# Kernel optimization log

Measured on AMD Instinct MI355X. Metric: run time of the kernel, lower is better.

## Reference

```python
import jax, jax.numpy as jnp
import numpy as np

N = 100000   # nodes
E = 1600000  # edges
D_IN = 128
H = 64
L = 3        # num SAGE layers
G = 512      # graphs in batch


def setup_inputs() -> dict:
    key = jax.random.key(0)
    ks = jax.random.split(key, 12)
    s = 0.05
    return {
        "x": jax.random.normal(ks[0], (N, D_IN), dtype=jnp.float32),
        "edge_index": jax.random.randint(ks[1], (2, E), 0, N, dtype=jnp.int64),
        "edge_attr": jax.random.normal(ks[2], (E, 1), dtype=jnp.float32),
        "batch": jnp.sort(jax.random.randint(ks[3], (N,), 0, G, dtype=jnp.int64)),
        "W0": jax.random.normal(ks[4], (D_IN, H), dtype=jnp.float32) * s,
        "b0": jnp.zeros((H,), dtype=jnp.float32),
        "Wl": jax.random.normal(ks[5], (L, H, H), dtype=jnp.float32) * s,  # lin_l (aggregated neighbors), has bias
        "bl": jnp.zeros((L, H), dtype=jnp.float32),
        "Wr": jax.random.normal(ks[6], (L, H, H), dtype=jnp.float32) * s,  # lin_r (root), no bias
        "W1": jax.random.normal(ks[7], (H, H), dtype=jnp.float32) * s,
        "b1": jnp.zeros((H,), dtype=jnp.float32),
    }


def reference(x, edge_index, edge_attr, batch, W0, b0, Wl, bl, Wr, W1, b1):
    # edge_attr is accepted but unused, matching the torch module.
    h = jax.nn.relu(x @ W0 + b0)                    # [N, H]
    src, dst = edge_index[0], edge_index[1]
    ones_e = jnp.ones((E,), dtype=h.dtype)
    deg = jax.ops.segment_sum(ones_e, dst, num_segments=N)
    deg = jnp.clip(deg, 1.0)[:, None]               # avoid div by zero (PyG mean -> 0 for isolated)
    for i in range(L):
        # SAGEConv: mean-aggregate source features onto targets, then lin_l(agg)+lin_r(h)
        agg = jax.ops.segment_sum(h[src], dst, num_segments=N) / deg  # [N, H]
        h = jax.nn.relu(agg @ Wl[i] + bl[i] + h @ Wr[i])
    # global_mean_pool over batch ids
    cnt = jax.ops.segment_sum(jnp.ones((N,), dtype=h.dtype), batch, num_segments=G)
    pooled = jax.ops.segment_sum(h, batch, num_segments=G) / jnp.clip(cnt, 1.0)[:, None]  # [G, H]
    return pooled @ W1 + b1                          # [G, H]
```

## Files before the change

### kernel.cpp

```cpp
#include <hip/hip_runtime.h>
#include <hip/hip_bf16.h>

#define NN 100000
#define NE 1600000
#define DIN 128
#define NG 512
#define MAXD 64
#define NBUK 391
#define BCAP 5120
#define CHUNK ((NE + NBUK - 1) / NBUK)
#define NTILE ((NN + 63) >> 6)

typedef __attribute__((ext_vector_type(8))) __bf16 bf16x8;
typedef __attribute__((ext_vector_type(4))) float f32x4;

static __device__ __forceinline__ unsigned short bfhi(float f) {
    __hip_bfloat16 h = __float2bfloat16(f);
    return *reinterpret_cast<unsigned short*>(&h);
}
static __device__ __forceinline__ float bf2f(unsigned short u) {
    unsigned v = (unsigned)u << 16;
    return __uint_as_float(v);
}
static __device__ __forceinline__ bf16x8 ldfrag(const void* p) {
    bf16x8 r;
    __builtin_memcpy(&r, p, 16);
    return r;
}
static __device__ __forceinline__ int swz(int a) {
    return a ^ (((a >> 8) & 3) << 5) ^ (((a >> 12) & 3) << 4);
}


#define GB 256
__global__ void __launch_bounds__(512) k_front(const int* __restrict__ src,
                                               const int* __restrict__ dst,
                                               int* __restrict__ cursor,
                                               unsigned int* __restrict__ bucket,
                                               const float* __restrict__ x,
                                               const float* __restrict__ W0,
                                               const float* __restrict__ b0,
                                               float* __restrict__ h) {
    __shared__ unsigned short sA0[16 * 64 * 8];
    __shared__ unsigned short sA1[16 * 64 * 8];
    __shared__ unsigned short sB0[16 * 64 * 8];
    __shared__ unsigned short sB1[16 * 64 * 8];
    __shared__ int lcnt[NBUK];
    __shared__ int lbase[NBUK];
    if (blockIdx.x < NBUK) {
        for (int i = threadIdx.x; i < NBUK; i += 512) lcnt[i] = 0;
        __syncthreads();
        int e0 = blockIdx.x * CHUNK;
        int e1 = min(e0 + CHUNK, NE);
        for (int e = e0 + (int)threadIdx.x; e < e1; e += 512)
            atomicAdd(&lcnt[dst[e] >> 8], 1);
        __syncthreads();
        for (int i = threadIdx.x; i < NBUK; i += 512) {
            int c = lcnt[i];
            lbase[i] = c ? atomicAdd(&cursor[i], c) : 0;
            lcnt[i] = 0;
        }
        __syncthreads();
        for (int e = e0 + (int)threadIdx.x; e < e1; e += 512) {
            int d = dst[e];
            int s = src[e];
            int bk = d >> 8;
            int pos = lbase[bk] + atomicAdd(&lcnt[bk], 1);
            if (pos < BCAP)
                bucket[(size_t)bk * BCAP + pos] = ((unsigned)s << 8) | (unsigned)(d & 255);
        }
    } else {
        for (int i = threadIdx.x; i < 8192; i += 512) {
            int k = i >> 6, c = i & 63;
            int slot = ((k >> 5) << 2) | (c >> 4);
            int ln   = (((k >> 3) & 3) << 4) | (c & 15);
            int ba   = swz((((((slot << 6) | ln) << 3) | (k & 7)) << 1));
            float w0 = W0[i];
            unsigned short hh = bfhi(w0);
            *(unsigned short*)((char*)sB0 + ba) = hh;
            *(unsigned short*)((char*)sB1 + ba) = bfhi(w0 - bf2f(hh));
        }
        int lane = threadIdx.x & 63;
        int wv   = threadIdx.x >> 6;
        int cb   = wv & 3;
        int rbh  = wv >> 2;
        int col  = (cb << 4) | (lane & 15);
        float bj = b0[col];
        int r0   = (lane >> 4) << 2;
        for (int t = blockIdx.x - NBUK; t < NTILE; t += GB) {
            int n0 = t << 6;
            __syncthreads();
#pragma unroll
            for (int i = 0; i < 4; ++i) {
                int tau = (int)threadIdx.x + (i << 9);
                int r = tau >> 5, kq = tau & 31;
                int n = n0 + r;
                float4 v = make_float4(0.f, 0.f, 0.f, 0.f);
                if (n < NN) v = *(const float4*)(x + ((size_t)n << 7) + (kq << 2));
                int k0   = kq << 2;
                int slot = ((k0 >> 5) << 2) | (r >> 4);
                int ln   = (((k0 >> 3) & 3) << 4) | (r & 15);
                int ba   = swz((((((slot << 6) | ln) << 3) | (k0 & 7)) << 1));
                unsigned short h0 = bfhi(v.x), h1 = bfhi(v.y),
                               h2 = bfhi(v.z), h3 = bfhi(v.w);
                *(ushort4*)((char*)sA0 + ba) = make_ushort4(h0, h1, h2, h3);
                *(ushort4*)((char*)sA1 + ba) = make_ushort4(
                    bfhi(v.x - bf2f(h0)), bfhi(v.y - bf2f(h1)),
                    bfhi(v.z - bf2f(h2)), bfhi(v.w - bf2f(h3)));
            }
            __syncthreads();
            f32x4 acc[2] = {{0.f,0.f,0.f,0.f},{0.f,0.f,0.f,0.f}};
#pragma unroll
            for (int ks = 0; ks < 4; ++ks) {
                int bb = swz(((((ks << 2) | cb) << 6) | lane) << 4);
                bf16x8 bh  = ldfrag((const char*)sB0 + bb);
                bf16x8 bl_ = ldfrag((const char*)sB1 + bb);
#pragma unroll
                for (int rl = 0; rl < 2; ++rl) {
                    int rb = (rbh << 1) | rl;
                    int ab = swz(((((ks << 2) | rb) << 6) | lane) << 4);
                    bf16x8 ah = ldfrag((const char*)sA0 + ab);
                    bf16x8 al = ldfrag((const char*)sA1 + ab);
                    acc[rl] = __builtin_amdgcn_mfma_f32_16x16x32_bf16(ah, bh,  acc[rl], 0, 0, 0);
                    acc[rl] = __builtin_amdgcn_mfma_f32_16x16x32_bf16(ah, bl_, acc[rl], 0, 0, 0);
                    acc[rl] = __builtin_amdgcn_mfma_f32_16x16x32_bf16(al, bh,  acc[rl], 0, 0, 0);
                }
            }
#pragma unroll
            for (int rl = 0; rl < 2; ++rl) {
                int rb = (rbh << 1) | rl;
#pragma unroll
                for (int reg = 0; reg < 4; ++reg) {
                    int row = (rb << 4) + r0 + reg;
                    int n = n0 + row;
                    if (n < NN)
                        h[((size_t)n << 6) + col] = fmaxf(acc[rl][reg] + bj, 0.f);
                }
            }
        }
    }
}

__device__ __forceinline__ void gemmLR_mfma(unsigned short* sA0, unsigned short* sA1,
                                            unsigned short* sBL0, unsigned short* sBL1,
                                            unsigned short* sBR0, unsigned short* sBR1,
                                            int tid, int nblk, int bidx,
                                            float* __restrict__ h_r,
                                            __hip_bfloat16* __restrict__ g,
                                            const float* __restrict__ Wl,
                                            const float* __restrict__ bl,
                                            const float* __restrict__ Wr) {
    for (int i = tid; i < 4096; i += 256) {
        int k = i >> 6, c = i & 63;
        int slot = ((k >> 5) << 2) | (c >> 4);
        int ln   = (((k >> 3) & 3) << 4) | (c & 15);
        int ba   = swz((((((slot << 6) | ln) << 3) | (k & 7)) << 1));
        float wl = Wl[i];
        unsigned short hl = bfhi(wl);
        *(unsigned short*)((char*)sBL0 + ba) = hl;
        *(unsigned short*)((char*)sBL1 + ba) = bfhi(wl - bf2f(hl));
        float wr = Wr[i];
        unsigned short hr = bfhi(wr);
        *(unsigned short*)((char*)sBR0 + ba) = hr;
        *(unsigned short*)((char*)sBR1 + ba) = bfhi(wr - bf2f(hr));
    }
    int lane = tid & 63;
    int cb   = tid >> 6;
    int col  = (cb << 4) | (lane & 15);
    float bj = bl[col];
    int r0   = (lane >> 4) << 2;
    unsigned short* gp = (unsigned short*)g;
    for (int t = bidx; t < NTILE; t += nblk) {
        int n0 = t << 6;
        __syncthreads();
#pragma unroll
        for (int i = 0; i < 4; ++i) {
            int tau = tid + (i << 8);
            int r = tau >> 4, kq = tau & 15;
            int n = n0 + r;
            float4 v = make_float4(0.f, 0.f, 0.f, 0.f);
            if (n < NN) v = *(const float4*)(h_r + ((size_t)n << 6) + (kq << 2));
            int k0   = kq << 2;
            int slot = ((k0 >> 5) << 2) | (r >> 4);
            int ln   = (((k0 >> 3) & 3) << 4) | (r & 15);
            int ba   = swz((((((slot << 6) | ln) << 3) | (k0 & 7)) << 1));
            unsigned short h0 = bfhi(v.x), h1 = bfhi(v.y),
                           h2 = bfhi(v.z), h3 = bfhi(v.w);
            *(ushort4*)((char*)sA0 + ba) = make_ushort4(h0, h1, h2, h3);
            *(ushort4*)((char*)sA1 + ba) = make_ushort4(
                bfhi(v.x - bf2f(h0)), bfhi(v.y - bf2f(h1)),
                bfhi(v.z - bf2f(h2)), bfhi(v.w - bf2f(h3)));
        }
        __syncthreads();
        f32x4 accl[4] = {{0.f,0.f,0.f,0.f},{0.f,0.f,0.f,0.f},
                         {0.f,0.f,0.f,0.f},{0.f,0.f,0.f,0.f}};
        f32x4 accr[4] = {{0.f,0.f,0.f,0.f},{0.f,0.f,0.f,0.f},
                         {0.f,0.f,0.f,0.f},{0.f,0.f,0.f,0.f}};
#pragma unroll
        for (int ks = 0; ks < 2; ++ks) {
            int bb = swz(((((ks << 2) | cb) << 6) | lane) << 4);
            bf16x8 bLh = ldfrag((const char*)sBL0 + bb);
            bf16x8 bLl = ldfrag((const char*)sBL1 + bb);
            bf16x8 bRh = ldfrag((const char*)sBR0 + bb);
            bf16x8 bRl = ldfrag((const char*)sBR1 + bb);
#pragma unroll
            for (int rb = 0; rb < 4; ++rb) {
                int ab = swz(((((ks << 2) | rb) << 6) | lane) << 4);
                bf16x8 ah = ldfrag((const char*)sA0 + ab);
                bf16x8 al = ldfrag((const char*)sA1 + ab);
                accl[rb] = __builtin_amdgcn_mfma_f32_16x16x32_bf16(ah, bLh, accl[rb], 0, 0, 0);
                accl[rb] = __builtin_amdgcn_mfma_f32_16x16x32_bf16(ah, bLl, accl[rb], 0, 0, 0);
                accl[rb] = __builtin_amdgcn_mfma_f32_16x16x32_bf16(al, bLh, accl[rb], 0, 0, 0);
                accr[rb] = __builtin_amdgcn_mfma_f32_16x16x32_bf16(ah, bRh, accr[rb], 0, 0, 0);
                accr[rb] = __builtin_amdgcn_mfma_f32_16x16x32_bf16(ah, bRl, accr[rb], 0, 0, 0);
                accr[rb] = __builtin_amdgcn_mfma_f32_16x16x32_bf16(al, bRh, accr[rb], 0, 0, 0);
            }
        }
#pragma unroll
        for (int rb = 0; rb < 4; ++rb) {
#pragma unroll
            for (int reg = 0; reg < 4; ++reg) {
                int row = (rb << 4) + r0 + reg;
                int n = n0 + row;
                if (n < NN) {
                    size_t o = ((size_t)n << 6) + col;
                    gp[o]  = bfhi(accl[rb][reg]);
                    h_r[o] = accr[rb][reg] + bj;
                }
            }
        }
    }
}

#define MGB 512
__global__ void __launch_bounds__(256) k_mid(const unsigned int* __restrict__ bucket,
                                             const int* __restrict__ cursor,
                                             int* __restrict__ cnt,
                                             int* __restrict__ ell,
                                             float* __restrict__ h_r,
                                             __hip_bfloat16* __restrict__ g,
                                             const float* __restrict__ Wl,
                                             const float* __restrict__ bl,
                                             const float* __restrict__ Wr) {
    __shared__ unsigned short sA0[8 * 64 * 8];
    __shared__ unsigned short sA1[8 * 64 * 8];
    __shared__ unsigned short sBL0[8 * 64 * 8];
    __shared__ unsigned short sBL1[8 * 64 * 8];
    __shared__ unsigned short sBR0[8 * 64 * 8];
    __shared__ unsigned short sBR1[8 * 64 * 8];
    __shared__ int lc[256];
    if (blockIdx.x < NBUK) {
        lc[threadIdx.x] = 0;
        int b = blockIdx.x;
        int4* ep = (int4*)(ell + (((size_t)b << 8) * MAXD));
        for (int i = threadIdx.x; i < (256 * MAXD) / 4; i += 256)
            ep[i] = make_int4(NN, NN, NN, NN);
        __syncthreads();
        int m = min(cursor[b], BCAP);
        const unsigned int* bp = bucket + (size_t)b * BCAP;
        for (int i = threadIdx.x; i < m; i += 256) {
            unsigned v = bp[i];
            int dlo = (int)(v & 255u);
            int s   = (int)(v >> 8);
            int p   = atomicAdd(&lc[dlo], 1);
            if (p < MAXD)
                ell[(((size_t)b << 8) + dlo) * MAXD + p] = s;
        }
        __syncthreads();
        int n = (b << 8) + (int)threadIdx.x;
        if (n < NN) cnt[n] = lc[threadIdx.x];
    } else {
        gemmLR_mfma(sA0, sA1, sBL0, sBL1, sBR0, sBR1,
                    threadIdx.x, MGB, blockIdx.x - NBUK, h_r, g, Wl, bl, Wr);
    }
}

__global__ void __launch_bounds__(256) k_gemmLR(float* __restrict__ h_r,
                                                __hip_bfloat16* __restrict__ g,
                                                const float* __restrict__ Wl,
                                                const float* __restrict__ bl,
                                                const float* __restrict__ Wr) {
    __shared__ unsigned short sA0[8 * 64 * 8];
    __shared__ unsigned short sA1[8 * 64 * 8];
    __shared__ unsigned short sBL0[8 * 64 * 8];
    __shared__ unsigned short sBL1[8 * 64 * 8];
    __shared__ unsigned short sBR0[8 * 64 * 8];
    __shared__ unsigned short sBR1[8 * 64 * 8];
    gemmLR_mfma(sA0, sA1, sBL0, sBL1, sBR0, sBR1,
                threadIdx.x, gridDim.x, blockIdx.x, h_r, g, Wl, bl, Wr);
}

__global__ void __launch_bounds__(256) k_gather(const uint2* __restrict__ g2,
                                                float* __restrict__ r_h,
                                                const int* __restrict__ cnt,
                                                const int* __restrict__ ell) {
    int lane = threadIdx.x & 63;
    int q    = lane >> 4;
    int c16  = lane & 15;
    int wv = __builtin_amdgcn_readfirstlane((int)((blockIdx.x * 256 + threadIdx.x) >> 6));
    int nw = (gridDim.x * 256) >> 6;
    for (int p = wv; p < NN / 4; p += nw) {
        int n0  = 4 * p;
        int myn = n0 + q;
        int d   = cnt[myn];
        int dm  = max(d, __shfl_xor(d, 16));
        dm      = max(dm, __shfl_xor(dm, 32));
        int maxd  = min(dm, MAXD);
        int iters = (maxd + 7) & ~7;
        int4 ld = *(const int4*)(ell + ((size_t)myn << 6) + (c16 << 2));
        float a0=0.f, a1=0.f, a2=0.f, a3=0.f;
        float e0=0.f, e1=0.f, e2=0.f, e3=0.f;
        for (int j0 = 0; j0 < iters; j0 += 8) {
            int s0 = (q << 4) | (j0 >> 2);
            int i0 = __shfl(ld.x, s0);
            int i1 = __shfl(ld.y, s0);
            int i2 = __shfl(ld.z, s0);
            int i3 = __shfl(ld.w, s0);
            int i4 = __shfl(ld.x, s0 + 1);
            int i5 = __shfl(ld.y, s0 + 1);
            int i6 = __shfl(ld.z, s0 + 1);
            int i7 = __shfl(ld.w, s0 + 1);
            uint2 u0 = g2[(size_t)i0 * 16 + c16];
            uint2 u1 = g2[(size_t)i1 * 16 + c16];
            uint2 u2 = g2[(size_t)i2 * 16 + c16];
            uint2 u3 = g2[(size_t)i3 * 16 + c16];
            uint2 u4 = g2[(size_t)i4 * 16 + c16];
            uint2 u5 = g2[(size_t)i5 * 16 + c16];
            uint2 u6 = g2[(size_t)i6 * 16 + c16];
            uint2 u7 = g2[(size_t)i7 * 16 + c16];
            a0 += __uint_as_float(u0.x << 16); a1 += __uint_as_float(u0.x & 0xffff0000u);
            a2 += __uint_as_float(u0.y << 16); a3 += __uint_as_float(u0.y & 0xffff0000u);
            e0 += __uint_as_float(u1.x << 16); e1 += __uint_as_float(u1.x & 0xffff0000u);
            e2 += __uint_as_float(u1.y << 16); e3 += __uint_as_float(u1.y & 0xffff0000u);
            a0 += __uint_as_float(u2.x << 16); a1 += __uint_as_float(u2.x & 0xffff0000u);
            a2 += __uint_as_float(u2.y << 16); a3 += __uint_as_float(u2.y & 0xffff0000u);
            e0 += __uint_as_float(u3.x << 16); e1 += __uint_as_float(u3.x & 0xffff0000u);
            e2 += __uint_as_float(u3.y << 16); e3 += __uint_as_float(u3.y & 0xffff0000u);
            a0 += __uint_as_float(u4.x << 16); a1 += __uint_as_float(u4.x & 0xffff0000u);
            a2 += __uint_as_float(u4.y << 16); a3 += __uint_as_float(u4.y & 0xffff0000u);
            e0 += __uint_as_float(u5.x << 16); e1 += __uint_as_float(u5.x & 0xffff0000u);
            e2 += __uint_as_float(u5.y << 16); e3 += __uint_as_float(u5.y & 0xffff0000u);
            a0 += __uint_as_float(u6.x << 16); a1 += __uint_as_float(u6.x & 0xffff0000u);
            a2 += __uint_as_float(u6.y << 16); a3 += __uint_as_float(u6.y & 0xffff0000u);
            e0 += __uint_as_float(u7.x << 16); e1 += __uint_as_float(u7.x & 0xffff0000u);
            e2 += __uint_as_float(u7.y << 16); e3 += __uint_as_float(u7.y & 0xffff0000u);
        }
        float inv = 1.0f / fmaxf((float)d, 1.0f);
        float4* rp = (float4*)r_h + ((size_t)myn << 4) + c16;
        float4 rv = *rp;
        rv.x = fmaxf(fmaf(a0 + e0, inv, rv.x), 0.0f);
        rv.y = fmaxf(fmaf(a1 + e1, inv, rv.y), 0.0f);
        rv.z = fmaxf(fmaf(a2 + e2, inv, rv.z), 0.0f);
        rv.w = fmaxf(fmaf(a3 + e3, inv, rv.w), 0.0f);
        *rp = rv;
    }
}

__global__ void __launch_bounds__(256) k_pool(const int* __restrict__ batch,
                                              const float* __restrict__ h,
                                              float* __restrict__ pool,
                                              float* __restrict__ cntg) {
    int lane = threadIdx.x & 63;
    int wid  = (blockIdx.x * 256 + threadIdx.x) >> 6;
    int nw   = (gridDim.x * 256) >> 6;
    int chunk = (NN + nw - 1) / nw;
    int n0 = wid * chunk;
    if (n0 >= NN) return;
    int n1 = min(n0 + chunk, NN);
    int cur = batch[n0];
    float acc = 0.0f, acc_c = 0.0f;
    for (int n = n0; n < n1; ++n) {
        int b = batch[n];
        if (b != cur) {
            atomicAdd(&pool[(size_t)cur * 64 + lane], acc);
            if (lane == 0) atomicAdd(&cntg[cur], acc_c);
            acc = 0.0f; acc_c = 0.0f; cur = b;
        }
        acc   += h[(size_t)n * 64 + lane];
        acc_c += 1.0f;
    }
    atomicAdd(&pool[(size_t)cur * 64 + lane], acc);
    if (lane == 0) atomicAdd(&cntg[cur], acc_c);
}

__global__ void __launch_bounds__(256) k_out(const float* __restrict__ pool,
                                             const float* __restrict__ cntg,
                                             const float* __restrict__ W1,
                                             const float* __restrict__ b1,
                                             float* __restrict__ out) {
    __shared__ float sW[64 * 64];
    for (int i = threadIdx.x; i < 64 * 64; i += 256) sW[i] = W1[i];
    __syncthreads();
    int lane = threadIdx.x & 63;
    int wid  = (blockIdx.x * 256 + threadIdx.x) >> 6;
    int nw   = (gridDim.x * 256) >> 6;
    for (int gidx = wid; gidx < NG; gidx += nw) {
        float ic = 1.0f / fmaxf(cntg[gidx], 1.0f);
        float acc = 0.0f;
#pragma unroll
        for (int k = 0; k < 64; ++k)
            acc = fmaf(pool[(size_t)gidx * 64 + k], sW[k * 64 + lane], acc);
        out[(size_t)gidx * 64 + lane] = fmaf(acc, ic, b1[lane]);
    }
}

extern "C" void kernel_launch(void* const* d_in, const int* in_sizes, int n_in,
                              void* d_out, int out_size, void* d_ws, size_t ws_size,
                              hipStream_t stream) {
    const float* x     = (const float*)d_in[0];
    const int*   ei    = (const int*)d_in[1];
    const int*   batch = (const int*)d_in[3];
    const float* W0    = (const float*)d_in[4];
    const float* b0    = (const float*)d_in[5];
    const float* Wl    = (const float*)d_in[6];
    const float* bl    = (const float*)d_in[7];
    const float* Wr    = (const float*)d_in[8];
    const float* W1    = (const float*)d_in[9];
    const float* b1    = (const float*)d_in[10];
    float* out = (float*)d_out;

    char* ws = (char*)d_ws;
    size_t off = 0;
    auto alloc = [&](size_t bytes) -> void* {
        void* p = ws + off;
        off += (bytes + 255) & ~(size_t)255;
        return p;
    };
    float*          A      = (float*)alloc((size_t)NN * 64 * 4);
    __hip_bfloat16* G      = (__hip_bfloat16*)alloc((size_t)NN * 64 * 2);
    size_t zstart = off;
    (void)alloc((size_t)MAXD * 2);
    int*   cursor = (int*)alloc((size_t)NBUK * 4);
    float* pool   = (float*)alloc((size_t)NG * 64 * 4);
    float* cntg   = (float*)alloc((size_t)NG * 4);
    size_t zlen = off - zstart;
    int*          ell    = (int*)alloc((size_t)NBUK * 256 * MAXD * 4);
    unsigned int* bucket = (unsigned int*)alloc((size_t)NBUK * BCAP * 4);
    int*          cnt    = (int*)alloc((size_t)NN * 4);

    const int* src = ei;
    const int* dst = ei + NE;

    hipMemsetAsync(ws + zstart, 0, zlen, stream);

    k_front<<<NBUK + GB, 512, 0, stream>>>(src, dst, cursor, bucket, x, W0, b0, A);
    k_mid<<<NBUK + MGB, 256, 0, stream>>>(bucket, cursor, cnt, ell, A, G,
                                          Wl, bl, Wr);
    k_gather<<<4096, 256, 0, stream>>>((const uint2*)G, A, cnt, ell);

    for (int l = 1; l < 3; ++l) {
        k_gemmLR<<<512, 256, 0, stream>>>(A, G,
                                          Wl + (size_t)l * 64 * 64,
                                          bl + (size_t)l * 64,
                                          Wr + (size_t)l * 64 * 64);
        k_gather<<<4096, 256, 0, stream>>>((const uint2*)G, A, cnt, ell);
    }

    k_pool<<<256, 256, 0, stream>>>(batch, A, pool, cntg);
    k_out<<<128, 256, 0, stream>>>(pool, cntg, W1, b1, out);
}
```

Before: 394.2 us.

## Hold weight fragments in registers, shrink LDS, widen gather to 8 nodes per wave

The GEMM kernels now load the split-bf16 weight fragments from LDS into registers once, then reuse a single shared buffer pair for activation tiles. This cuts LDS footprint, which may allow more resident blocks. The neighbor gather now handles 8 nodes per wave, with 16-byte loads per lane and software prefetch of the next batch of 8 neighbor rows. The aim is more memory-level parallelism in the bandwidth-bound gather, at the cost of higher register pressure and a smaller grid.

```diff
diff --git a/kernel.cpp b/kernel.cpp
--- a/kernel.cpp
+++ b/kernel.cpp
@@ -41,10 +41,7 @@
                                                const float* __restrict__ W0,
                                                const float* __restrict__ b0,
                                                float* __restrict__ h) {
-    __shared__ unsigned short sA0[16 * 64 * 8];
-    __shared__ unsigned short sA1[16 * 64 * 8];
-    __shared__ unsigned short sB0[16 * 64 * 8];
-    __shared__ unsigned short sB1[16 * 64 * 8];
+    __shared__ unsigned short sS[2 * 8192];
     __shared__ int lcnt[NBUK];
     __shared__ int lbase[NBUK];
     if (blockIdx.x < NBUK) {
@@ -70,6 +67,8 @@
                 bucket[(size_t)bk * BCAP + pos] = ((unsigned)s << 8) | (unsigned)(d & 255);
         }
     } else {
+        unsigned short* sP0 = sS;
+        unsigned short* sP1 = sS + 8192;
         for (int i = threadIdx.x; i < 8192; i += 512) {
             int k = i >> 6, c = i & 63;
             int slot = ((k >> 5) << 2) | (c >> 4);
@@ -77,9 +76,10 @@
             int ba   = swz((((((slot << 6) | ln) << 3) | (k & 7)) << 1));
             float w0 = W0[i];
             unsigned short hh = bfhi(w0);
-            *(unsigned short*)((char*)sB0 + ba) = hh;
-            *(unsigned short*)((char*)sB1 + ba) = bfhi(w0 - bf2f(hh));
-        }
+            *(unsigned short*)((char*)sP0 + ba) = hh;
+            *(unsigned short*)((char*)sP1 + ba) = bfhi(w0 - bf2f(hh));
+        }
+        __syncthreads();
         int lane = threadIdx.x & 63;
         int wv   = threadIdx.x >> 6;
         int cb   = wv & 3;
@@ -87,6 +87,13 @@
         int col  = (cb << 4) | (lane & 15);
         float bj = b0[col];
         int r0   = (lane >> 4) << 2;
+        bf16x8 Bh[4], Bl[4];
+#pragma unroll
+        for (int ks = 0; ks < 4; ++ks) {
+            int bb = swz(((((ks << 2) | cb) << 6) | lane) << 4);
+            Bh[ks] = ldfrag((const char*)sP0 + bb);
+            Bl[ks] = ldfrag((const char*)sP1 + bb);
+        }
         for (int t = blockIdx.x - NBUK; t < NTILE; t += GB) {
             int n0 = t << 6;
             __syncthreads();
@@ -103,8 +110,8 @@
                 int ba   = swz((((((slot << 6) | ln) << 3) | (k0 & 7)) << 1));
                 unsigned short h0 = bfhi(v.x), h1 = bfhi(v.y),
                                h2 = bfhi(v.z), h3 = bfhi(v.w);
-                *(ushort4*)((char*)sA0 + ba) = make_ushort4(h0, h1, h2, h3);
-                *(ushort4*)((char*)sA1 + ba) = make_ushort4(
+                *(ushort4*)((char*)sP0 + ba) = make_ushort4(h0, h1, h2, h3);
+                *(ushort4*)((char*)sP1 + ba) = make_ushort4(
                     bfhi(v.x - bf2f(h0)), bfhi(v.y - bf2f(h1)),
                     bfhi(v.z - bf2f(h2)), bfhi(v.w - bf2f(h3)));
             }
@@ -112,18 +119,15 @@
             f32x4 acc[2] = {{0.f,0.f,0.f,0.f},{0.f,0.f,0.f,0.f}};
 #pragma unroll
             for (int ks = 0; ks < 4; ++ks) {
-                int bb = swz(((((ks << 2) | cb) << 6) | lane) << 4);
-                bf16x8 bh  = ldfrag((const char*)sB0 + bb);
-                bf16x8 bl_ = ldfrag((const char*)sB1 + bb);
 #pragma unroll
                 for (int rl = 0; rl < 2; ++rl) {
                     int rb = (rbh << 1) | rl;
                     int ab = swz(((((ks << 2) | rb) << 6) | lane) << 4);
-                    bf16x8 ah = ldfrag((const char*)sA0 + ab);
-                    bf16x8 al = ldfrag((const char*)sA1 + ab);
-                    acc[rl] = __builtin_amdgcn_mfma_f32_16x16x32_bf16(ah, bh,  acc[rl], 0, 0, 0);
-                    acc[rl] = __builtin_amdgcn_mfma_f32_16x16x32_bf16(ah, bl_, acc[rl], 0, 0, 0);
-                    acc[rl] = __builtin_amdgcn_mfma_f32_16x16x32_bf16(al, bh,  acc[rl], 0, 0, 0);
+                    bf16x8 ah = ldfrag((const char*)sP0 + ab);
+                    bf16x8 al = ldfrag((const char*)sP1 + ab);
+                    acc[rl] = __builtin_amdgcn_mfma_f32_16x16x32_bf16(ah, Bh[ks], acc[rl], 0, 0, 0);
+                    acc[rl] = __builtin_amdgcn_mfma_f32_16x16x32_bf16(ah, Bl[ks], acc[rl], 0, 0, 0);
+                    acc[rl] = __builtin_amdgcn_mfma_f32_16x16x32_bf16(al, Bh[ks], acc[rl], 0, 0, 0);
                 }
             }
 #pragma unroll
@@ -141,34 +145,56 @@
     }
 }
 
-__device__ __forceinline__ void gemmLR_mfma(unsigned short* sA0, unsigned short* sA1,
-                                            unsigned short* sBL0, unsigned short* sBL1,
-                                            unsigned short* sBR0, unsigned short* sBR1,
+__device__ __forceinline__ void gemmLR_mfma(unsigned short* sS,
                                             int tid, int nblk, int bidx,
                                             float* __restrict__ h_r,
                                             __hip_bfloat16* __restrict__ g,
                                             const float* __restrict__ Wl,
                                             const float* __restrict__ bl,
                                             const float* __restrict__ Wr) {
+    unsigned short* sP0 = sS;
+    unsigned short* sP1 = sS + 4096;
+    int lane = tid & 63;
+    int cb   = tid >> 6;
+    bf16x8 BLh[2], BLl[2], BRh[2], BRl[2];
     for (int i = tid; i < 4096; i += 256) {
         int k = i >> 6, c = i & 63;
         int slot = ((k >> 5) << 2) | (c >> 4);
         int ln   = (((k >> 3) & 3) << 4) | (c & 15);
         int ba   = swz((((((slot << 6) | ln) << 3) | (k & 7)) << 1));
-        float wl = Wl[i];
-        unsigned short hl = bfhi(wl);
-        *(unsigned short*)((char*)sBL0 + ba) = hl;
-        *(unsigned short*)((char*)sBL1 + ba) = bfhi(wl - bf2f(hl));
-        float wr = Wr[i];
-        unsigned short hr = bfhi(wr);
-        *(unsigned short*)((char*)sBR0 + ba) = hr;
-        *(unsigned short*)((char*)sBR1 + ba) = bfhi(wr - bf2f(hr));
-    }
-    int lane = tid & 63;
-    int cb   = tid >> 6;
-    int col  = (cb << 4) | (lane & 15);
+        float w = Wl[i];
+        unsigned short hh = bfhi(w);
+        *(unsigned short*)((char*)sP0 + ba) = hh;
+        *(unsigned short*)((char*)sP1 + ba) = bfhi(w - bf2f(hh));
+    }
+    __syncthreads();
+#pragma unroll
+    for (int ks = 0; ks < 2; ++ks) {
+        int bb = swz(((((ks << 2) | cb) << 6) | lane) << 4);
+        BLh[ks] = ldfrag((const char*)sP0 + bb);
+        BLl[ks] = ldfrag((const char*)sP1 + bb);
+    }
+    __syncthreads();
+    for (int i = tid; i < 4096; i += 256) {
+        int k = i >> 6, c = i & 63;
+        int slot = ((k >> 5) << 2) | (c >> 4);
+        int ln   = (((k >> 3) & 3) << 4) | (c & 15);
+        int ba   = swz((((((slot << 6) | ln) << 3) | (k & 7)) << 1));
+        float w = Wr[i];
+        unsigned short hh = bfhi(w);
+        *(unsigned short*)((char*)sP0 + ba) = hh;
+        *(unsigned short*)((char*)sP1 + ba) = bfhi(w - bf2f(hh));
+    }
+    __syncthreads();
+#pragma unroll
+    for (int ks = 0; ks < 2; ++ks) {
+        int bb = swz(((((ks << 2) | cb) << 6) | lane) << 4);
+        BRh[ks] = ldfrag((const char*)sP0 + bb);
+        BRl[ks] = ldfrag((const char*)sP1 + bb);
+    }
+    int col = (cb << 4) | (lane & 15);
     float bj = bl[col];
-    int r0   = (lane >> 4) << 2;
+    int r0  = (lane >> 4) << 2;
     unsigned short* gp = (unsigned short*)g;
     for (int t = bidx; t < NTILE; t += nblk) {
         int n0 = t << 6;
@@ -186,8 +212,8 @@
             int ba   = swz((((((slot << 6) | ln) << 3) | (k0 & 7)) << 1));
             unsigned short h0 = bfhi(v.x), h1 = bfhi(v.y),
                            h2 = bfhi(v.z), h3 = bfhi(v.w);
-            *(ushort4*)((char*)sA0 + ba) = make_ushort4(h0, h1, h2, h3);
-            *(ushort4*)((char*)sA1 + ba) = make_ushort4(
+            *(ushort4*)((char*)sP0 + ba) = make_ushort4(h0, h1, h2, h3);
+            *(ushort4*)((char*)sP1 + ba) = make_ushort4(
                 bfhi(v.x - bf2f(h0)), bfhi(v.y - bf2f(h1)),
                 bfhi(v.z - bf2f(h2)), bfhi(v.w - bf2f(h3)));
         }
@@ -198,22 +224,17 @@
                          {0.f,0.f,0.f,0.f},{0.f,0.f,0.f,0.f}};
 #pragma unroll
         for (int ks = 0; ks < 2; ++ks) {
-            int bb = swz(((((ks << 2) | cb) << 6) | lane) << 4);
-            bf16x8 bLh = ldfrag((const char*)sBL0 + bb);
-            bf16x8 bLl = ldfrag((const char*)sBL1 + bb);
-            bf16x8 bRh = ldfrag((const char*)sBR0 + bb);
-            bf16x8 bRl = ldfrag((const char*)sBR1 + bb);
 #pragma unroll
             for (int rb = 0; rb < 4; ++rb) {
                 int ab = swz(((((ks << 2) | rb) << 6) | lane) << 4);
-                bf16x8 ah = ldfrag((const char*)sA0 + ab);
-                bf16x8 al = ldfrag((const char*)sA1 + ab);
-                accl[rb] = __builtin_amdgcn_mfma_f32_16x16x32_bf16(ah, bLh, accl[rb], 0, 0, 0);
-                accl[rb] = __builtin_amdgcn_mfma_f32_16x16x32_bf16(ah, bLl, accl[rb], 0, 0, 0);
-                accl[rb] = __builtin_amdgcn_mfma_f32_16x16x32_bf16(al, bLh, accl[rb], 0, 0, 0);
-                accr[rb] = __builtin_amdgcn_mfma_f32_16x16x32_bf16(ah, bRh, accr[rb], 0, 0, 0);
-                accr[rb] = __builtin_amdgcn_mfma_f32_16x16x32_bf16(ah, bRl, accr[rb], 0, 0, 0);
-                accr[rb] = __builtin_amdgcn_mfma_f32_16x16x32_bf16(al, bRh, accr[rb], 0, 0, 0);
+                bf16x8 ah = ldfrag((const char*)sP0 + ab);
+                bf16x8 al = ldfrag((const char*)sP1 + ab);
+                accl[rb] = __builtin_amdgcn_mfma_f32_16x16x32_bf16(ah, BLh[ks], accl[rb], 0, 0, 0);
+                accl[rb] = __builtin_amdgcn_mfma_f32_16x16x32_bf16(ah, BLl[ks], accl[rb], 0, 0, 0);
+                accl[rb] = __builtin_amdgcn_mfma_f32_16x16x32_bf16(al, BLh[ks], accl[rb], 0, 0, 0);
+                accr[rb] = __builtin_amdgcn_mfma_f32_16x16x32_bf16(ah, BRh[ks], accr[rb], 0, 0, 0);
+                accr[rb] = __builtin_amdgcn_mfma_f32_16x16x32_bf16(ah, BRl[ks], accr[rb], 0, 0, 0);
+                accr[rb] = __builtin_amdgcn_mfma_f32_16x16x32_bf16(al, BRh[ks], accr[rb], 0, 0, 0);
             }
         }
 #pragma unroll
@@ -242,12 +263,7 @@
                                              const float* __restrict__ Wl,
                                              const float* __restrict__ bl,
                                              const float* __restrict__ Wr) {
-    __shared__ unsigned short sA0[8 * 64 * 8];
-    __shared__ unsigned short sA1[8 * 64 * 8];
-    __shared__ unsigned short sBL0[8 * 64 * 8];
-    __shared__ unsigned short sBL1[8 * 64 * 8];
-    __shared__ unsigned short sBR0[8 * 64 * 8];
-    __shared__ unsigned short sBR1[8 * 64 * 8];
+    __shared__ unsigned short sS[2 * 4096];
     __shared__ int lc[256];
     if (blockIdx.x < NBUK) {
         lc[threadIdx.x] = 0;
@@ -270,8 +286,7 @@
         int n = (b << 8) + (int)threadIdx.x;
         if (n < NN) cnt[n] = lc[threadIdx.x];
     } else {
-        gemmLR_mfma(sA0, sA1, sBL0, sBL1, sBR0, sBR1,
-                    threadIdx.x, MGB, blockIdx.x - NBUK, h_r, g, Wl, bl, Wr);
+        gemmLR_mfma(sS, threadIdx.x, MGB, blockIdx.x - NBUK, h_r, g, Wl, bl, Wr);
     }
 }
 
@@ -280,79 +295,75 @@
                                                 const float* __restrict__ Wl,
                                                 const float* __restrict__ bl,
                                                 const float* __restrict__ Wr) {
-    __shared__ unsigned short sA0[8 * 64 * 8];
-    __shared__ unsigned short sA1[8 * 64 * 8];
-    __shared__ unsigned short sBL0[8 * 64 * 8];
-    __shared__ unsigned short sBL1[8 * 64 * 8];
-    __shared__ unsigned short sBR0[8 * 64 * 8];
-    __shared__ unsigned short sBR1[8 * 64 * 8];
-    gemmLR_mfma(sA0, sA1, sBL0, sBL1, sBR0, sBR1,
-                threadIdx.x, gridDim.x, blockIdx.x, h_r, g, Wl, bl, Wr);
-}
-
-__global__ void __launch_bounds__(256) k_gather(const uint2* __restrict__ g2,
+    __shared__ unsigned short sS[2 * 4096];
+    gemmLR_mfma(sS, threadIdx.x, gridDim.x, blockIdx.x, h_r, g, Wl, bl, Wr);
+}
+
+#define ACCU(U) { \
+    a0 += __uint_as_float((U).x << 16); a1 += __uint_as_float((U).x & 0xffff0000u); \
+    a2 += __uint_as_float((U).y << 16); a3 += __uint_as_float((U).y & 0xffff0000u); \
+    a4 += __uint_as_float((U).z << 16); a5 += __uint_as_float((U).z & 0xffff0000u); \
+    a6 += __uint_as_float((U).w << 16); a7 += __uint_as_float((U).w & 0xffff0000u); }
+__global__ void __launch_bounds__(256) k_gather(const uint4* __restrict__ g4,
                                                 float* __restrict__ r_h,
                                                 const int* __restrict__ cnt,
                                                 const int* __restrict__ ell) {
     int lane = threadIdx.x & 63;
-    int q    = lane >> 4;
-    int c16  = lane & 15;
+    int o    = lane >> 3;
+    int c8   = lane & 7;
     int wv = __builtin_amdgcn_readfirstlane((int)((blockIdx.x * 256 + threadIdx.x) >> 6));
     int nw = (gridDim.x * 256) >> 6;
-    for (int p = wv; p < NN / 4; p += nw) {
-        int n0  = 4 * p;
-        int myn = n0 + q;
+    for (int p = wv; p < NN / 8; p += nw) {
+        int myn = 8 * p + o;
         int d   = cnt[myn];
-        int dm  = max(d, __shfl_xor(d, 16));
+        int dm  = max(d, __shfl_xor(d, 8));
+        dm      = max(dm, __shfl_xor(dm, 16));
         dm      = max(dm, __shfl_xor(dm, 32));
-        int maxd  = min(dm, MAXD);
-        int iters = (maxd + 7) & ~7;
-        int4 ld = *(const int4*)(ell + ((size_t)myn << 6) + (c16 << 2));
-        float a0=0.f, a1=0.f, a2=0.f, a3=0.f;
-        float e0=0.f, e1=0.f, e2=0.f, e3=0.f;
-        for (int j0 = 0; j0 < iters; j0 += 8) {
-            int s0 = (q << 4) | (j0 >> 2);
-            int i0 = __shfl(ld.x, s0);
-            int i1 = __shfl(ld.y, s0);
-            int i2 = __shfl(ld.z, s0);
-            int i3 = __shfl(ld.w, s0);
-            int i4 = __shfl(ld.x, s0 + 1);
-            int i5 = __shfl(ld.y, s0 + 1);
-            int i6 = __shfl(ld.z, s0 + 1);
-            int i7 = __shfl(ld.w, s0 + 1);
-            uint2 u0 = g2[(size_t)i0 * 16 + c16];
-            uint2 u1 = g2[(size_t)i1 * 16 + c16];
-            uint2 u2 = g2[(size_t)i2 * 16 + c16];
-            uint2 u3 = g2[(size_t)i3 * 16 + c16];
-            uint2 u4 = g2[(size_t)i4 * 16 + c16];
-            uint2 u5 = g2[(size_t)i5 * 16 + c16];
-            uint2 u6 = g2[(size_t)i6 * 16 + c16];
-            uint2 u7 = g2[(size_t)i7 * 16 + c16];
-            a0 += __uint_as_float(u0.x << 16); a1 += __uint_as_float(u0.x & 0xffff0000u);
-            a2 += __uint_as_float(u0.y << 16); a3 += __uint_as_float(u0.y & 0xffff0000u);
-            e0 += __uint_as_float(u1.x << 16); e1 += __uint_as_float(u1.x & 0xffff0000u);
-            e2 += __uint_as_float(u1.y << 16); e3 += __uint_as_float(u1.y & 0xffff0000u);
-            a0 += __uint_as_float(u2.x << 16); a1 += __uint_as_float(u2.x & 0xffff0000u);
-            a2 += __uint_as_float(u2.y << 16); a3 += __uint_as_float(u2.y & 0xffff0000u);
-            e0 += __uint_as_float(u3.x << 16); e1 += __uint_as_float(u3.x & 0xffff0000u);
-            e2 += __uint_as_float(u3.y << 16); e3 += __uint_as_float(u3.y & 0xffff0000u);
-            a0 += __uint_as_float(u4.x << 16); a1 += __uint_as_float(u4.x & 0xffff0000u);
-            a2 += __uint_as_float(u4.y << 16); a3 += __uint_as_float(u4.y & 0xffff0000u);
-            e0 += __uint_as_float(u5.x << 16); e1 += __uint_as_float(u5.x & 0xffff0000u);
-            e2 += __uint_as_float(u5.y << 16); e3 += __uint_as_float(u5.y & 0xffff0000u);
-            a0 += __uint_as_float(u6.x << 16); a1 += __uint_as_float(u6.x & 0xffff0000u);
-            a2 += __uint_as_float(u6.y << 16); a3 += __uint_as_float(u6.y & 0xffff0000u);
-            e0 += __uint_as_float(u7.x << 16); e1 += __uint_as_float(u7.x & 0xffff0000u);
-            e2 += __uint_as_float(u7.y << 16); e3 += __uint_as_float(u7.y & 0xffff0000u);
+        int iters = (min(dm, MAXD) + 7) & ~7;
+        const int* er = ell + ((size_t)myn << 6) + (c8 << 3);
+        int4 l0 = *(const int4*)er;
+        int4 l1 = *(const int4*)(er + 4);
+        float a0=0.f,a1=0.f,a2=0.f,a3=0.f,a4=0.f,a5=0.f,a6=0.f,a7=0.f;
+        if (iters > 0) {
+            int sl = o << 3;
+            uint4 c0 = g4[(size_t)__shfl(l0.x, sl) * 8 + c8];
+            uint4 c1 = g4[(size_t)__shfl(l0.y, sl) * 8 + c8];
+            uint4 c2 = g4[(size_t)__shfl(l0.z, sl) * 8 + c8];
+            uint4 c3 = g4[(size_t)__shfl(l0.w, sl) * 8 + c8];
+            uint4 c4 = g4[(size_t)__shfl(l1.x, sl) * 8 + c8];
+            uint4 c5 = g4[(size_t)__shfl(l1.y, sl) * 8 + c8];
+            uint4 c6 = g4[(size_t)__shfl(l1.z, sl) * 8 + c8];
+            uint4 c7 = g4[(size_t)__shfl(l1.w, sl) * 8 + c8];
+            for (int j0 = 8; j0 < iters; j0 += 8) {
+                int s2 = (o << 3) | (j0 >> 3);
+                uint4 n0v = g4[(size_t)__shfl(l0.x, s2) * 8 + c8];
+                uint4 n1v = g4[(size_t)__shfl(l0.y, s2) * 8 + c8];
+                uint4 n2v = g4[(size_t)__shfl(l0.z, s2) * 8 + c8];
+                uint4 n3v = g4[(size_t)__shfl(l0.w, s2) * 8 + c8];
+                uint4 n4v = g4[(size_t)__shfl(l1.x, s2) * 8 + c8];
+                uint4 n5v = g4[(size_t)__shfl(l1.y, s2) * 8 + c8];
+                uint4 n6v = g4[(size_t)__shfl(l1.z, s2) * 8 + c8];
+                uint4 n7v = g4[(size_t)__shfl(l1.w, s2) * 8 + c8];
+                ACCU(c0); ACCU(c1); ACCU(c2); ACCU(c3);
+                ACCU(c4); ACCU(c5); ACCU(c6); ACCU(c7);
+                c0 = n0v; c1 = n1v; c2 = n2v; c3 = n3v;
+                c4 = n4v; c5 = n5v; c6 = n6v; c7 = n7v;
+            }
+            ACCU(c0); ACCU(c1); ACCU(c2); ACCU(c3);
+            ACCU(c4); ACCU(c5); ACCU(c6); ACCU(c7);
         }
         float inv = 1.0f / fmaxf((float)d, 1.0f);
-        float4* rp = (float4*)r_h + ((size_t)myn << 4) + c16;
-        float4 rv = *rp;
-        rv.x = fmaxf(fmaf(a0 + e0, inv, rv.x), 0.0f);
-        rv.y = fmaxf(fmaf(a1 + e1, inv, rv.y), 0.0f);
-        rv.z = fmaxf(fmaf(a2 + e2, inv, rv.z), 0.0f);
-        rv.w = fmaxf(fmaf(a3 + e3, inv, rv.w), 0.0f);
-        *rp = rv;
+        float4* rp = (float4*)(r_h + ((size_t)myn << 6) + (c8 << 3));
+        float4 rv0 = rp[0], rv1 = rp[1];
+        rv0.x = fmaxf(fmaf(a0, inv, rv0.x), 0.0f);
+        rv0.y = fmaxf(fmaf(a1, inv, rv0.y), 0.0f);
+        rv0.z = fmaxf(fmaf(a2, inv, rv0.z), 0.0f);
+        rv0.w = fmaxf(fmaf(a3, inv, rv0.w), 0.0f);
+        rv1.x = fmaxf(fmaf(a4, inv, rv1.x), 0.0f);
+        rv1.y = fmaxf(fmaf(a5, inv, rv1.y), 0.0f);
+        rv1.z = fmaxf(fmaf(a6, inv, rv1.z), 0.0f);
+        rv1.w = fmaxf(fmaf(a7, inv, rv1.w), 0.0f);
+        rp[0] = rv0; rp[1] = rv1;
     }
 }
 
@@ -446,14 +457,14 @@
     k_front<<<NBUK + GB, 512, 0, stream>>>(src, dst, cursor, bucket, x, W0, b0, A);
     k_mid<<<NBUK + MGB, 256, 0, stream>>>(bucket, cursor, cnt, ell, A, G,
                                           Wl, bl, Wr);
-    k_gather<<<4096, 256, 0, stream>>>((const uint2*)G, A, cnt, ell);
+    k_gather<<<3200, 256, 0, stream>>>((const uint4*)G, A, cnt, ell);
 
     for (int l = 1; l < 3; ++l) {
         k_gemmLR<<<512, 256, 0, stream>>>(A, G,
                                           Wl + (size_t)l * 64 * 64,
                                           bl + (size_t)l * 64,
                                           Wr + (size_t)l * 64 * 64);
-        k_gather<<<4096, 256, 0, stream>>>((const uint2*)G, A, cnt, ell);
+        k_gather<<<3200, 256, 0, stream>>>((const uint4*)G, A, cnt, ell);
     }
 
     k_pool<<<256, 256, 0, stream>>>(batch, A, pool, cntg);
```

After: 407.6 us. +3.4%, slower.
